# Kernel tuning notes

Hardware: AMD Instinct MI355X
Metric: run time of the kernel (lower is better)

Reference implementation:

```python
import jax, jax.numpy as jnp
import numpy as np

C = 256


def conv2d(x, w, b, stride=1, groups=1, pad=1):
    out = jax.lax.conv_general_dilated(
        x, w, (stride, stride), ((pad, pad), (pad, pad)),
        feature_group_count=groups,
        dimension_numbers=('NCHW', 'OIHW', 'NCHW'))
    return out + b[None, :, None, None]


def dwconv(x, dwW, dwB, pwW, pwB, stride=1):
    # YOLOX-style DWConv: depthwise 3x3 (+SiLU) then pointwise 1x1 (+SiLU); BN folded into bias.
    x = jax.nn.silu(conv2d(x, dwW, dwB, stride=stride, groups=x.shape[1], pad=1))
    return jax.nn.silu(conv2d(x, pwW, pwB, stride=1, groups=1, pad=0))


def resize_bilinear_ac(x, Ho, Wo):
    # bilinear with align_corners=True (semantics of F.upsample_bilinear)
    _, _, h, w = x.shape
    ys = jnp.linspace(0.0, h - 1.0, Ho)
    xs = jnp.linspace(0.0, w - 1.0, Wo)
    y0 = jnp.floor(ys).astype(jnp.int32); y1 = jnp.minimum(y0 + 1, h - 1)
    x0 = jnp.floor(xs).astype(jnp.int32); x1 = jnp.minimum(x0 + 1, w - 1)
    wy = (ys - y0)[None, None, :, None]
    wx = (xs - x0)[None, None, None, :]
    rows = x[:, :, y0, :] * (1.0 - wy) + x[:, :, y1, :] * wy
    return rows[:, :, :, x0] * (1.0 - wx) + rows[:, :, :, x1] * wx


def h_sigmoid(x):
    return jnp.clip(x + 3.0, 0.0, 6.0) / 6.0


def attn_branch(fea, aw, ab):
    # AdaptiveAvgPool2d(1) -> 1x1 conv (C->1) -> ReLU, shape [B,1,1,1]
    m = fea.mean((2, 3))                              # [B,C]
    a = jax.nn.relu(m @ aw.reshape(1, -1).T + ab)     # [B,1]
    return a[:, :, None, None]


def maxpool3x3(x):
    # 3x3 spatial max pool, stride 1, pad 1 (-inf padding like torch MaxPool)
    return jax.lax.reduce_window(x, -jnp.inf, jax.lax.max,
                                 (1, 1, 3, 3), (1, 1, 1, 1),
                                 ((0, 0), (0, 0), (1, 1), (1, 1)))


def fuse(branches, aw, ab):
    # attention-weight each branch, max over branches, then 3x3 spatial max
    # (equals MaxPool3d(kernel=(n_branch,3,3), pad=(0,1,1)) on stacked tensor)
    weighted = jnp.stack([f * h_sigmoid(attn_branch(f, aw, ab)) for f in branches])
    return maxpool3x3(weighted.max(0))


def dyrelu(x, w1, b1, w2, b2):
    # DyHead DYReLU with lambda_a=1.0 (=> *2), init_a=[1,0], init_b=[0,0]
    y = x.mean((2, 3))                                # [B,C]
    y = jax.nn.relu(y @ w1.T + b1)
    y = h_sigmoid(y @ w2.T + b2)                      # [B,4C]
    a1, bb1, a2, bb2 = jnp.split(y, 4, axis=1)
    a1 = (a1 - 0.5) * 2.0 + 1.0
    a2 = (a2 - 0.5) * 2.0
    bb1 = bb1 - 0.5
    bb2 = bb2 - 0.5
    e = lambda t: t[:, :, None, None]
    return jnp.maximum(x * e(a1) + e(bb1), x * e(a2) + e(bb2))


def setup_inputs() -> dict:
    key = jax.random.key(0)
    ks = jax.random.split(key, 12)
    B = 8
    inp = {
        'x0': jax.random.normal(ks[0], (B, C, 64, 64), jnp.float32),
        'x1': jax.random.normal(ks[1], (B, C, 32, 32), jnp.float32),
        'x2': jax.random.normal(ks[2], (B, C, 16, 16), jnp.float32),
        # 9 DWConvs (3 per level); weights init N(0, 0.01), biases zero per init_weights
        'dw_w': jax.random.normal(ks[3], (9, C, 1, 3, 3), jnp.float32) * 0.01,
        'dw_b': jnp.zeros((9, C), jnp.float32),
        'pw_w': jax.random.normal(ks[4], (9, C, C, 1, 1), jnp.float32) * 0.01,
        'pw_b': jnp.zeros((9, C), jnp.float32),
        'attn_w': jax.random.normal(ks[5], (1, C, 1, 1), jnp.float32) * 0.01,
        'attn_b': jnp.zeros((1,), jnp.float32),
        # DYReLU FCs: squeeze = C // 4
        'fc1_w': jax.random.normal(ks[6], (C // 4, C), jnp.float32) * 0.01,
        'fc1_b': jnp.zeros((C // 4,), jnp.float32),
        'fc2_w': jax.random.normal(ks[7], (4 * C, C // 4), jnp.float32) * 0.01,
        'fc2_b': jnp.zeros((4 * C,), jnp.float32),
    }
    return inp


def reference(x0, x1, x2, dw_w, dw_b, pw_w, pw_b, attn_w, attn_b,
              fc1_w, fc1_b, fc2_w, fc2_b):
    dc = lambda i, x, s=1: dwconv(x, dw_w[i], dw_b[i], pw_w[i], pw_b[i], stride=s)

    def level(branches):
        return dyrelu(fuse(branches, attn_w, attn_b), fc1_w, fc1_b, fc2_w, fc2_b)

    # level 0: own conv + upsampled next level (both use DyConv[3*0+1], as in source)
    b0 = [dc(1, x0), resize_bilinear_ac(dc(1, x1), x0.shape[2], x0.shape[3])]
    # level 1: own + stride-2 conv of prev + upsampled next
    b1 = [dc(4, x1), dc(5, x0, 2), resize_bilinear_ac(dc(4, x2), x1.shape[2], x1.shape[3])]
    # level 2 (last): own + stride-2 conv of prev
    b2 = [dc(7, x2), dc(8, x1, 2)]
    return (level(b0), level(b1), level(b2))
```

## Files before the change

### kernel.cpp

```cpp
#include <hip/hip_runtime.h>

#define BB 8
#define CC 256

typedef __attribute__((ext_vector_type(8))) short short8;
typedef __attribute__((ext_vector_type(4))) float f32x4;

__device__ __forceinline__ float silu_f(float v){ return v / (1.f + expf(-v)); }
__device__ __forceinline__ float hsig_f(float v){ return fminf(fmaxf(v + 3.f, 0.f), 6.f) * (1.f/6.f); }
__device__ __forceinline__ unsigned short f2bf(float f){
  unsigned int u = __float_as_uint(f);
  unsigned int r = u + 0x7fffu + ((u >> 16) & 1u);
  return (unsigned short)(r >> 16);
}
__device__ __forceinline__ float bf2f(unsigned short u){ return __uint_as_float(((unsigned int)u)<<16); }

struct DwG {
  const float* in;
  const float* w1a; const float* b1a; unsigned short* o1a;
  const float* w1b; const float* b1b; unsigned short* o1b;
  const float* w2;  const float* b2;  unsigned short* o2;
  int blocks;
};
struct DwPrepArgs {
  DwG g[3];
  const float* pw_w; unsigned short* wbf;
  float* wtab32; float* wtab16; float* zeros;
};

template<int C> struct RowT { float v[C+2]; };

template<int C>
__device__ __forceinline__ void loadRow(const float* rp, bool valid, bool hasL, bool hasR, RowT<C>& r){
  if (!valid){
    #pragma unroll
    for (int i=0;i<C+2;++i) r.v[i]=0.f;
    return;
  }
  r.v[0] = hasL ? rp[-1] : 0.f;
  #pragma unroll
  for (int q=0;q<C/4;++q){
    float4 f = *(const float4*)(rp + q*4);
    r.v[1+q*4+0]=f.x; r.v[1+q*4+1]=f.y; r.v[1+q*4+2]=f.z; r.v[1+q*4+3]=f.w;
  }
  r.v[C+1] = hasR ? rp[C] : 0.f;
}

template<int C>
__device__ __forceinline__ void conv1row(const RowT<C>& ra, const RowT<C>& rb, const RowT<C>& rc,
                                         const float* w9, float bias, unsigned short* dst){
  #pragma unroll
  for (int j=0;j<C;++j){
    float a = bias
      + w9[0]*ra.v[j] + w9[1]*ra.v[j+1] + w9[2]*ra.v[j+2]
      + w9[3]*rb.v[j] + w9[4]*rb.v[j+1] + w9[5]*rb.v[j+2]
      + w9[6]*rc.v[j] + w9[7]*rc.v[j+1] + w9[8]*rc.v[j+2];
    dst[j] = f2bf(silu_f(a));
  }
}

template<int C>
__device__ __forceinline__ void conv1rowS2(const RowT<C>& ra, const RowT<C>& rb, const RowT<C>& rc,
                                           const float* w9, float bias, unsigned short* dst){
  #pragma unroll
  for (int jj=0;jj<C/2;++jj){
    float a = bias
      + w9[0]*ra.v[2*jj] + w9[1]*ra.v[2*jj+1] + w9[2]*ra.v[2*jj+2]
      + w9[3]*rb.v[2*jj] + w9[4]*rb.v[2*jj+1] + w9[5]*rb.v[2*jj+2]
      + w9[6]*rc.v[2*jj] + w9[7]*rc.v[2*jj+1] + w9[8]*rc.v[2*jj+2];
    dst[jj] = f2bf(silu_f(a));
  }
}

template<int LWO, int RO, int P>
__device__ __forceinline__ void writeFrag(const unsigned short* sbuf, unsigned short* outBase,
                                          int cg, int tid){
  constexpr int WO = 1<<LWO;
  constexpr int iters = (RO*WO*8)/256;
  #pragma unroll
  for (int h=0; h<iters; ++h){
    int jc = h*256 + tid;
    int lp = jc & 15, c8 = (jc>>4)&7, ptl = jc>>7;
    int pl = ptl*16 + lp;
    int rowl = pl >> LWO, col = pl & (WO-1);
    const unsigned short* sp = sbuf + ((size_t)(c8*8)*RO + rowl)*P + col;
    unsigned int e0 = sp[0*RO*P], e1 = sp[1*RO*P], e2 = sp[2*RO*P], e3 = sp[3*RO*P];
    unsigned int e4 = sp[4*RO*P], e5 = sp[5*RO*P], e6 = sp[6*RO*P], e7 = sp[7*RO*P];
    uint4 v;
    v.x = e0 | (e1<<16); v.y = e2 | (e3<<16); v.z = e4 | (e5<<16); v.w = e6 | (e7<<16);
    size_t off = (size_t)ptl*4096 + (size_t)(cg*2 + (c8>>2))*512 + (c8&3)*128 + lp*8;
    *(uint4*)(outBase + off) = v;
  }
}

template<int LW, int R, int N1, bool S2>
__device__ void dw_group(const DwG& g, int bid, unsigned short* sm){
  constexpr int W = 1<<LW;
  constexpr int C = W/4;
  constexpr int P1 = W + 4;
  constexpr int P2 = W/2 + 4;
  const int tid = threadIdx.x;
  const int ch = tid >> 2, ct = tid & 3, c0 = ct*C;
  const int cg = bid & 3;
  int rest = bid >> 2;
  const int NR = W / R;
  const int b = rest / NR, rb = rest % NR, r0 = rb * R;

  const float* ip = g.in + ((size_t)b*CC + cg*64 + ch) * (W*W);
  const int chg = cg*64 + ch;
  float w1a[9], w1b[9], w2[9];
  float bs1a = g.b1a[chg], bs1b = 0.f, bs2 = 0.f;
  #pragma unroll
  for (int k=0;k<9;++k) w1a[k] = g.w1a[chg*9+k];
  if (N1==2){
    bs1b = g.b1b[chg];
    #pragma unroll
    for (int k=0;k<9;++k) w1b[k] = g.w1b[chg*9+k];
  }
  if (S2){
    bs2 = g.b2[chg];
    #pragma unroll
    for (int k=0;k<9;++k) w2[k] = g.w2[chg*9+k];
  }

  unsigned short* s1a = sm;
  unsigned short* s1b = sm + (size_t)64*R*P1;
  unsigned short* s2b = sm + (size_t)N1*64*R*P1;

  RowT<C> RA, RB, RC;
  const bool hasL = (c0 > 0), hasR = (c0 + C < W);
  {
    int ry = r0-1; loadRow<C>(ip + ry*W + c0, ry>=0 && ry<W, hasL, hasR, RA);
    ry = r0;       loadRow<C>(ip + ry*W + c0, ry>=0 && ry<W, hasL, hasR, RB);
    ry = r0+1;     loadRow<C>(ip + ry*W + c0, ry>=0 && ry<W, hasL, hasR, RC);
  }
  #pragma unroll
  for (int y=0; y<R; ++y){
    const RowT<C>& ra  = (y%3==0)?RA:((y%3==1)?RB:RC);
    const RowT<C>& rbm = (y%3==0)?RB:((y%3==1)?RC:RA);
    const RowT<C>& rc  = (y%3==0)?RC:((y%3==1)?RA:RB);
    conv1row<C>(ra, rbm, rc, w1a, bs1a, s1a + ((size_t)ch*R + y)*P1 + c0);
    if (N1==2) conv1row<C>(ra, rbm, rc, w1b, bs1b, s1b + ((size_t)ch*R + y)*P1 + c0);
    if (S2 && (y%2==0))
      conv1rowS2<C>(ra, rbm, rc, w2, bs2, s2b + ((size_t)ch*(R/2) + y/2)*P2 + c0/2);
    if (y < R-1){
      RowT<C>& dst = (y%3==0)?RA:((y%3==1)?RB:RC);
      int ry = r0 + y + 2;
      loadRow<C>(ip + ry*W + c0, ry>=0 && ry<W, hasL, hasR, dst);
    }
  }
  __syncthreads();

  {
    unsigned short* ob = g.o1a + ((size_t)b*(W*W) + r0*W)*256;
    writeFrag<LW, R, P1>(s1a, ob, cg, tid);
  }
  if (N1==2){
    unsigned short* ob = g.o1b + ((size_t)b*(W*W) + r0*W)*256;
    writeFrag<LW, R, P1>(s1b, ob, cg, tid);
  }
  if (S2){
    unsigned short* ob = g.o2 + ((size_t)b*((W/2)*(W/2)) + (r0/2)*(W/2))*256;
    writeFrag<LW-1, R/2, P2>(s2b, ob, cg, tid);
  }
}

__device__ float accw(int yi, int Ho, int Hi){
  float sc = (float)(Hi-1)/(float)(Ho-1);
  float a = 0.f;
  for (int yo=0; yo<Ho; ++yo){
    float ys = yo*sc; int y0 = (int)ys; float w = ys - y0; int y1 = min(y0+1, Hi-1);
    if (y0==yi) a += 1.f - w;
    if (y1==yi) a += w;
  }
  return a;
}

__global__ __launch_bounds__(256) void dw_kernel(DwPrepArgs A){
  __shared__ unsigned short smem[22016];
  int bid = blockIdx.x;
  if (bid < 832){
    int gi = 0;
    while (bid >= A.g[gi].blocks){ bid -= A.g[gi].blocks; ++gi; }
    if (gi == 0)      dw_group<6,4,1,true >(A.g[0], bid, smem);
    else if (gi == 1) dw_group<5,4,2,true >(A.g[1], bid, smem);
    else              dw_group<4,8,2,false>(A.g[2], bid, smem);
    return;
  }
  int idx = (bid - 832)*256 + threadIdx.x;
  const int T = 5*65536;
  if (idx < T){
    const int widx[5] = {1,4,5,7,8};
    int slot = idx >> 16, r = idx & 65535;
    int ct = r>>12, s=(r>>9)&7, g=(r>>7)&3, lr=(r>>3)&15, e=r&7;
    int co = ct*16+lr, k = s*32+g*8+e;
    A.wbf[idx] = f2bf(A.pw_w[(size_t)widx[slot]*65536 + co*256 + k]);
  } else if (idx < T+1024){
    int p = idx - T; int y=p>>5, x=p&31;
    A.wtab32[p] = accw(y,64,32)*accw(x,64,32);
  } else if (idx < T+1280){
    int p = idx - T - 1024; int y=p>>4, x=p&15;
    A.wtab16[p] = accw(y,32,16)*accw(x,32,16);
  } else if (idx < T+1280+20480){
    A.zeros[idx - T - 1280] = 0.f;
  }
}

struct PwT { const unsigned short* in; const unsigned short* w; const float* bias;
             unsigned short* out; const float* wtab; float norm; int HW; int blocks; int slot; };
struct PwArgs { PwT t[7]; };

__global__ __launch_bounds__(256) void pw_kernel(PwArgs A, float* __restrict__ means){
  __shared__ unsigned short cs[64*136];
  __shared__ float smean[64];
  int bid = blockIdx.x; int ti = 0;
  while (bid >= A.t[ti].blocks){ bid -= A.t[ti].blocks; ++ti; }
  PwT t = A.t[ti];
  const int nbx = t.HW >> 7;
  const int b  = bid / (nbx*4);
  const int r  = bid % (nbx*4);
  const int co0 = (r & 3) * 64;
  const int p0  = (r >> 2) * 128;
  const int tid = threadIdx.x;
  const int wid = tid >> 6, l = tid & 63;
  const int wm = wid >> 1, wn = wid & 1;
  const int lr = l & 15, g = l >> 4;

  if (tid < 64) smean[tid] = 0.f;

  const unsigned short* wbase = t.w + ((co0 + wm*32) >> 4)*4096 + l*8;
  const unsigned short* bbase = t.in + (size_t)b*t.HW*256 + ((p0 + wn*64) >> 4)*4096 + l*8;

  f32x4 acc[2][4] = {};
  #pragma unroll
  for (int s=0;s<8;++s){
    short8 av[2], bv[4];
    #pragma unroll
    for (int m=0;m<2;++m) av[m] = *(const short8*)(wbase + m*4096 + s*512);
    #pragma unroll
    for (int n=0;n<4;++n) bv[n] = *(const short8*)(bbase + n*4096 + s*512);
    #pragma unroll
    for (int m=0;m<2;++m){
      #pragma unroll
      for (int n=0;n<4;++n){
        acc[m][n] = __builtin_amdgcn_mfma_f32_16x16x32_bf16(av[m], bv[n], acc[m][n], 0,0,0);
      }
    }
  }

  float wgt[4];
  #pragma unroll
  for (int n=0;n<4;++n){
    int p = p0 + wn*64 + n*16 + lr;
    wgt[n] = t.wtab ? t.wtab[p] : 1.f;
  }

  __syncthreads();
  #pragma unroll
  for (int m=0;m<2;++m){
    #pragma unroll
    for (int rg=0;rg<4;++rg){
      int col = wm*32 + m*16 + g*4 + rg;
      float bias = t.bias[co0 + col];
      unsigned short* sp = cs + (size_t)col*136 + wn*64 + lr;
      float s = 0.f;
      #pragma unroll
      for (int n=0;n<4;++n){
        float v = silu_f(acc[m][n][rg] + bias);
        sp[n*16] = f2bf(v);
        s += v * wgt[n];
      }
      s += __shfl_xor(s, 1);
      s += __shfl_xor(s, 2);
      s += __shfl_xor(s, 4);
      s += __shfl_xor(s, 8);
      if (lr == 0) atomicAdd(&smean[col], s);
    }
  }
  __syncthreads();
  if (tid < 64){
    atomicAdd(&means[(size_t)t.slot*2048 + b*256 + co0 + tid], smean[tid] * t.norm);
  }
  #pragma unroll
  for (int h=0; h<4; ++h){
    int jc = h*256 + tid;
    int col = jc >> 4, pq = jc & 15;
    uint4 v = *(const uint4*)(cs + (size_t)col*136 + pq*8);
    unsigned short* op = t.out + ((size_t)(b*256 + co0 + col))*t.HW + p0 + pq*8;
    *(uint4*)op = v;
  }
}

struct FpT { const unsigned short* uA; const unsigned short* uB; const unsigned short* uUp;
             unsigned short* fea; int iA, iB, iUp, blocks; float norm; int lvl; };
struct FpArgs { FpT t[3]; };

template<int H, int LW, int SLAB, bool HASB, bool HASU, int HUP>
__device__ void fusepool_body(const FpT& t, int bid,
                              const float* __restrict__ means,
                              const float* __restrict__ atw, const float* __restrict__ atb,
                              float* __restrict__ feaMean, float* __restrict__ Vs){
  constexpr int W = 1 << LW;
  constexpr int P = W + 2;
  const int tid = threadIdx.x;
  const int bc = bid & 2047, si = bid >> 11;
  const int b = bc >> 8;
  const int r0 = si * SLAB;
  const unsigned short* pA = t.uA + (size_t)bc*H*W;
  const unsigned short* pB = HASB ? t.uB + (size_t)bc*H*W : nullptr;
  const unsigned short* pU = HASU ? t.uUp + (size_t)bc*HUP*HUP : nullptr;

  __shared__ float red4[4][3];
  __shared__ float atnL[3];
  {
    float awv = (tid < 256) ? atw[tid] : 0.f;
    float s0 = means[(size_t)t.iA*2048 + b*256 + tid] * awv;
    float s1 = HASB ? means[(size_t)t.iB*2048 + b*256 + tid] * awv : 0.f;
    float s2 = HASU ? means[(size_t)t.iUp*2048 + b*256 + tid] * awv : 0.f;
    #pragma unroll
    for (int off=32; off; off>>=1){
      s0 += __shfl_down(s0, off);
      if (HASB) s1 += __shfl_down(s1, off);
      if (HASU) s2 += __shfl_down(s2, off);
    }
    int wid = tid >> 6;
    if ((tid & 63) == 0){ red4[wid][0]=s0; red4[wid][1]=s1; red4[wid][2]=s2; }
    __syncthreads();
    if (tid == 0){
      float ab0 = atb[0];
      atnL[0] = hsig_f(fmaxf(red4[0][0]+red4[1][0]+red4[2][0]+red4[3][0] + ab0, 0.f));
      if (HASB) atnL[1] = hsig_f(fmaxf(red4[0][1]+red4[1][1]+red4[2][1]+red4[3][1] + ab0, 0.f));
      if (HASU) atnL[2] = hsig_f(fmaxf(red4[0][2]+red4[1][2]+red4[2][2]+red4[3][2] + ab0, 0.f));
    }
    __syncthreads();
  }
  const float wA = atnL[0];
  const float wB = HASB ? atnL[1] : 0.f;
  const float wU = HASU ? atnL[2] : 0.f;
  const float SC = HASU ? (float)(HUP-1)/(float)(H-1) : 0.f;

  for (int r=tid; r<SLAB+2; r+=256){ Vs[r*P] = -INFINITY; Vs[r*P + W+1] = -INFINITY; }

  constexpr int NQ = (SLAB+2)*(W/4);
  for (int q=tid; q<NQ; q+=256){
    int row = q >> (LW-2);
    int xq = (q & ((W/4)-1)) << 2;
    int y = r0 - 1 + row;
    float v0=-INFINITY, v1=-INFINITY, v2=-INFINITY, v3=-INFINITY;
    if (y >= 0 && y < H){
      int ro = y*W + xq;
      ushort4 a4 = *(const ushort4*)(pA + ro);
      v0 = bf2f(a4.x)*wA; v1 = bf2f(a4.y)*wA; v2 = bf2f(a4.z)*wA; v3 = bf2f(a4.w)*wA;
      if (HASB){
        ushort4 b4 = *(const ushort4*)(pB + ro);
        v0 = fmaxf(v0, bf2f(b4.x)*wB); v1 = fmaxf(v1, bf2f(b4.y)*wB);
        v2 = fmaxf(v2, bf2f(b4.z)*wB); v3 = fmaxf(v3, bf2f(b4.w)*wB);
      }
      if (HASU){
        float ys = y*SC; int y0 = (int)ys; float fy = ys - y0; int y1 = min(y0+1, HUP-1);
        const unsigned short* pu0 = pU + y0*HUP;
        const unsigned short* pu1 = pU + y1*HUP;
        float gy = 1.f - fy;
        #pragma unroll
        for (int j=0;j<4;++j){
          int x = xq + j;
          float xs = x*SC; int x0 = (int)xs; float fx = xs - x0; int x1 = min(x0+1, HUP-1);
          float gx = 1.f - fx;
          float ra = bf2f(pu0[x0])*gx + bf2f(pu0[x1])*fx;
          float rb = bf2f(pu1[x0])*gx + bf2f(pu1[x1])*fx;
          float uv = (ra*gy + rb*fy) * wU;
          if (j==0) v0 = fmaxf(v0, uv);
          else if (j==1) v1 = fmaxf(v1, uv);
          else if (j==2) v2 = fmaxf(v2, uv);
          else v3 = fmaxf(v3, uv);
        }
      }
    }
    float* vr = Vs + row*P + 1 + xq;
    vr[0]=v0; vr[1]=v1; vr[2]=v2; vr[3]=v3;
  }
  __syncthreads();

  float sum = 0.f;
  constexpr int NO = SLAB*(W/4);
  unsigned short* fb = t.fea + (size_t)bc*H*W + r0*W;
  for (int q=tid; q<NO; q+=256){
    int row = q >> (LW-2);
    int x4 = (q & ((W/4)-1)) << 2;
    const float* rp0 = Vs + row*P + x4;
    const float* rp1 = rp0 + P;
    const float* rp2 = rp1 + P;
    float c0,c1,c2,c3,c4,c5, m0,m1,m2,m3;
    c0=rp0[0]; c1=rp0[1]; c2=rp0[2]; c3=rp0[3]; c4=rp0[4]; c5=rp0[5];
    m0 = fmaxf(fmaxf(c0,c1),c2);
    m1 = fmaxf(fmaxf(c1,c2),c3);
    m2 = fmaxf(fmaxf(c2,c3),c4);
    m3 = fmaxf(fmaxf(c3,c4),c5);
    c0=rp1[0]; c1=rp1[1]; c2=rp1[2]; c3=rp1[3]; c4=rp1[4]; c5=rp1[5];
    m0 = fmaxf(m0, fmaxf(fmaxf(c0,c1),c2));
    m1 = fmaxf(m1, fmaxf(fmaxf(c1,c2),c3));
    m2 = fmaxf(m2, fmaxf(fmaxf(c2,c3),c4));
    m3 = fmaxf(m3, fmaxf(fmaxf(c3,c4),c5));
    c0=rp2[0]; c1=rp2[1]; c2=rp2[2]; c3=rp2[3]; c4=rp2[4]; c5=rp2[5];
    m0 = fmaxf(m0, fmaxf(fmaxf(c0,c1),c2));
    m1 = fmaxf(m1, fmaxf(fmaxf(c1,c2),c3));
    m2 = fmaxf(m2, fmaxf(fmaxf(c2,c3),c4));
    m3 = fmaxf(m3, fmaxf(fmaxf(c3,c4),c5));
    ushort4 o; o.x=f2bf(m0); o.y=f2bf(m1); o.z=f2bf(m2); o.w=f2bf(m3);
    *(ushort4*)(fb + row*W + x4) = o;
    sum += m0+m1+m2+m3;
  }
  #pragma unroll
  for (int off=32; off; off>>=1) sum += __shfl_down(sum, off);
  __shared__ float red[4];
  if ((tid & 63) == 0) red[tid >> 6] = sum;
  __syncthreads();
  if (tid == 0)
    atomicAdd(&feaMean[t.lvl*2048 + bc], (red[0]+red[1]+red[2]+red[3]) * t.norm);
}

__global__ __launch_bounds__(256) void fusepool_kernel(FpArgs A,
                                                       const float* __restrict__ means,
                                                       const float* __restrict__ atw,
                                                       const float* __restrict__ atb,
                                                       float* __restrict__ feaMean){
  __shared__ float Vs[34*66];
  int bid = blockIdx.x; int ti = 0;
  while (bid >= A.t[ti].blocks){ bid -= A.t[ti].blocks; ++ti; }
  if (ti == 0)      fusepool_body<64,6,32,false,true,32>(A.t[0], bid, means, atw, atb, feaMean, Vs);
  else if (ti == 1) fusepool_body<32,5,32,true, true,16>(A.t[1], bid, means, atw, atb, feaMean, Vs);
  else              fusepool_body<16,4,16,true,false, 2>(A.t[2], bid, means, atw, atb, feaMean, Vs);
}

__global__ __launch_bounds__(256) void fc_kernel(const float* __restrict__ feaMean,
                                                 const float* __restrict__ w1, const float* __restrict__ b1,
                                                 const float* __restrict__ w2, const float* __restrict__ b2,
                                                 float* __restrict__ coef){
  int lb = blockIdx.x;
  const float* m = feaMean + (size_t)lb*CC;
  __shared__ float sm[CC];
  __shared__ float sy[64];
  sm[threadIdx.x] = m[threadIdx.x];
  __syncthreads();
  if (threadIdx.x < 64){
    float s = b1[threadIdx.x];
    const float* wr = w1 + (size_t)threadIdx.x*CC;
    for (int k=0;k<CC;++k) s += wr[k]*sm[k];
    sy[threadIdx.x] = fmaxf(s, 0.f);
  }
  __syncthreads();
  for (int j = threadIdx.x; j < 1024; j += 256){
    float s = b2[j];
    const float* wr = w2 + (size_t)j*64;
    for (int k=0;k<64;++k) s += wr[k]*sy[k];
    float y = hsig_f(s);
    int seg = j >> 8;
    float o;
    if (seg==0)      o = (y-0.5f)*2.f + 1.f;
    else if (seg==1) o = y - 0.5f;
    else if (seg==2) o = (y-0.5f)*2.f;
    else             o = y - 0.5f;
    coef[(size_t)lb*1024 + j] = o;
  }
}

struct ApT { const unsigned short* fea; const float* coefL; float* out; int lhw; int blocks; };
struct ApArgs { ApT t[3]; };

__global__ __launch_bounds__(256) void apply_kernel(ApArgs A){
  int bid = blockIdx.x; int ti = 0;
  while (bid >= A.t[ti].blocks){ bid -= A.t[ti].blocks; ++ti; }
  ApT t = A.t[ti];
  int e0 = bid*2048 + threadIdx.x*8;
  int bc = e0 >> t.lhw;
  int b = bc >> 8, c = bc & 255;
  const float* cf = t.coefL + (size_t)b*1024;
  float a1 = cf[c], bb1 = cf[256+c], a2 = cf[512+c], bb2 = cf[768+c];
  uint4 xv = *(const uint4*)(t.fea + e0);
  float x0 = bf2f((unsigned short)(xv.x & 0xffff)), x1 = bf2f((unsigned short)(xv.x >> 16));
  float x2 = bf2f((unsigned short)(xv.y & 0xffff)), x3 = bf2f((unsigned short)(xv.y >> 16));
  float x4 = bf2f((unsigned short)(xv.z & 0xffff)), x5 = bf2f((unsigned short)(xv.z >> 16));
  float x6 = bf2f((unsigned short)(xv.w & 0xffff)), x7 = bf2f((unsigned short)(xv.w >> 16));
  float4 o0, o1;
  o0.x = fmaxf(x0*a1 + bb1, x0*a2 + bb2);
  o0.y = fmaxf(x1*a1 + bb1, x1*a2 + bb2);
  o0.z = fmaxf(x2*a1 + bb1, x2*a2 + bb2);
  o0.w = fmaxf(x3*a1 + bb1, x3*a2 + bb2);
  o1.x = fmaxf(x4*a1 + bb1, x4*a2 + bb2);
  o1.y = fmaxf(x5*a1 + bb1, x5*a2 + bb2);
  o1.z = fmaxf(x6*a1 + bb1, x6*a2 + bb2);
  o1.w = fmaxf(x7*a1 + bb1, x7*a2 + bb2);
  *(float4*)(t.out + e0) = o0;
  *(float4*)(t.out + e0 + 4) = o1;
}

extern "C" void kernel_launch(void* const* d_in, const int* in_sizes, int n_in,
                              void* d_out, int out_size, void* d_ws, size_t ws_size,
                              hipStream_t stream) {
  const float* x0    = (const float*)d_in[0];
  const float* x1    = (const float*)d_in[1];
  const float* x2    = (const float*)d_in[2];
  const float* dw_w  = (const float*)d_in[3];
  const float* dw_b  = (const float*)d_in[4];
  const float* pw_w  = (const float*)d_in[5];
  const float* pw_b  = (const float*)d_in[6];
  const float* atw   = (const float*)d_in[7];
  const float* atb   = (const float*)d_in[8];
  const float* fc1w  = (const float*)d_in[9];
  const float* fc1b  = (const float*)d_in[10];
  const float* fc2w  = (const float*)d_in[11];
  const float* fc2b  = (const float*)d_in[12];
  float* out = (float*)d_out;

  const size_t A64 = (size_t)BB*CC*64*64;
  const size_t A32 = (size_t)BB*CC*32*32;
  const size_t A16 = (size_t)BB*CC*16*16;

  unsigned short* us = (unsigned short*)d_ws;
  unsigned short* bA = us;
  unsigned short* bB = bA + A64;
  unsigned short* bC = bB + A32;
  unsigned short* bD = bC + A32;
  unsigned short* bE = bD + A32;
  unsigned short* bF = bE + A16;
  unsigned short* bG = bF + A16;
  unsigned short* uA = bG + A16;
  unsigned short* uB = uA + A64;
  unsigned short* uC = uB + A32;
  unsigned short* uD = uC + A32;
  unsigned short* uE = uD + A32;
  unsigned short* uF = uE + A16;
  unsigned short* uG = uF + A16;
  unsigned short* fe0 = uG + A16;
  unsigned short* fe1 = fe0 + A64;
  unsigned short* fe2 = fe1 + A32;
  unsigned short* wbf = fe2 + A16;
  float* fb      = (float*)(wbf + 5*65536);
  float* wtab32  = fb;
  float* wtab16  = wtab32 + 1024;
  float* means   = wtab16 + 256;
  float* feaMean = means + 7*2048;
  float* attnW   = feaMean + 3*2048;
  float* coef    = attnW + 64;

  const float* W1 = dw_w + 1*CC*9; const float* B1 = dw_b + 1*CC;
  const float* W4 = dw_w + 4*CC*9; const float* B4 = dw_b + 4*CC;
  const float* W5 = dw_w + 5*CC*9; const float* B5 = dw_b + 5*CC;
  const float* W7 = dw_w + 7*CC*9; const float* B7 = dw_b + 7*CC;
  const float* W8 = dw_w + 8*CC*9; const float* B8 = dw_b + 8*CC;

  {
    DwPrepArgs DA;
    DA.g[0] = {x0, W1,B1,bA,  nullptr,nullptr,nullptr,  W5,B5,bD,  512};
    DA.g[1] = {x1, W1,B1,bB,  W4,B4,bC,                 W8,B8,bG,  256};
    DA.g[2] = {x2, W4,B4,bE,  W7,B7,bF,                 nullptr,nullptr,nullptr, 64};
    DA.pw_w = pw_w; DA.wbf = wbf; DA.wtab32 = wtab32; DA.wtab16 = wtab16; DA.zeros = means;
    dw_kernel<<<832 + 1365, 256, 0, stream>>>(DA);
  }

  {
    PwArgs A;
    A.t[0] = {bA, wbf + 0*65536, pw_b + 1*CC, uA, nullptr, 1.f/4096.f, 4096, 1024, 0};
    A.t[1] = {bB, wbf + 0*65536, pw_b + 1*CC, uB, wtab32,  1.f/4096.f, 1024, 256, 1};
    A.t[2] = {bC, wbf + 1*65536, pw_b + 4*CC, uC, nullptr, 1.f/1024.f, 1024, 256, 2};
    A.t[3] = {bD, wbf + 2*65536, pw_b + 5*CC, uD, nullptr, 1.f/1024.f, 1024, 256, 3};
    A.t[4] = {bE, wbf + 1*65536, pw_b + 4*CC, uE, wtab16,  1.f/1024.f, 256,  64, 4};
    A.t[5] = {bF, wbf + 3*65536, pw_b + 7*CC, uF, nullptr, 1.f/256.f,  256,  64, 5};
    A.t[6] = {bG, wbf + 4*65536, pw_b + 8*CC, uG, nullptr, 1.f/256.f,  256,  64, 6};
    pw_kernel<<<1984, 256, 0, stream>>>(A, means);
  }

  {
    FpArgs F;
    F.t[0] = {uA, nullptr, uB,      fe0, 0,-1, 1, 4096, 1.f/4096.f, 0};
    F.t[1] = {uC, uD,      uE,      fe1, 2, 3, 4, 2048, 1.f/1024.f, 1};
    F.t[2] = {uF, uG,      nullptr, fe2, 5, 6,-1, 2048, 1.f/256.f,  2};
    fusepool_kernel<<<8192, 256, 0, stream>>>(F, means, atw, atb, feaMean);
  }

  fc_kernel<<<24, 256, 0, stream>>>(feaMean, fc1w, fc1b, fc2w, fc2b, coef);

  {
    ApArgs P;
    P.t[0] = {fe0, coef + 0*8192, out,             12, 4096};
    P.t[1] = {fe1, coef + 1*8192, out + A64,       10, 1024};
    P.t[2] = {fe2, coef + 2*8192, out + A64 + A32,  8, 256};
    apply_kernel<<<5376, 256, 0, stream>>>(P);
  }
}
```

Before: 128.5 us.

## Split depthwise conv blocks into 32-channel groups with 8 threads per channel row

The depthwise-conv stage now assigns 32 channels per block instead of 64, with 8 threads sharing each row instead of 4. This doubles the block count and halves shared memory per block, aiming for better occupancy and lower per-thread register pressure. The fragment writer is rewritten to pack the 32-channel half into the same blocked bf16 output layout. The cost is more halo loads per row and narrower per-thread work; for W=16, C=2 falls back to scalar loads.

```diff
diff --git a/kernel.cpp b/kernel.cpp
--- a/kernel.cpp
+++ b/kernel.cpp
@@ -38,10 +38,15 @@
     return;
   }
   r.v[0] = hasL ? rp[-1] : 0.f;
-  #pragma unroll
-  for (int q=0;q<C/4;++q){
-    float4 f = *(const float4*)(rp + q*4);
-    r.v[1+q*4+0]=f.x; r.v[1+q*4+1]=f.y; r.v[1+q*4+2]=f.z; r.v[1+q*4+3]=f.w;
+  if constexpr (C >= 4){
+    #pragma unroll
+    for (int q=0;q<C/4;++q){
+      float4 f = *(const float4*)(rp + q*4);
+      r.v[1+q*4+0]=f.x; r.v[1+q*4+1]=f.y; r.v[1+q*4+2]=f.z; r.v[1+q*4+3]=f.w;
+    }
+  } else {
+    #pragma unroll
+    for (int i=0;i<C;++i) r.v[1+i] = rp[i];
   }
   r.v[C+1] = hasR ? rp[C] : 0.f;
 }
@@ -73,41 +78,44 @@
 }
 
 template<int LWO, int RO, int P>
-__device__ __forceinline__ void writeFrag(const unsigned short* sbuf, unsigned short* outBase,
-                                          int cg, int tid){
+__device__ __forceinline__ void writeFrag32(const unsigned short* sbuf, unsigned short* outBase,
+                                            int cg, int tid){
   constexpr int WO = 1<<LWO;
-  constexpr int iters = (RO*WO*8)/256;
+  constexpr int total = RO*WO*4;
+  constexpr int iters = (total + 255)/256;
   #pragma unroll
   for (int h=0; h<iters; ++h){
     int jc = h*256 + tid;
-    int lp = jc & 15, c8 = (jc>>4)&7, ptl = jc>>7;
-    int pl = ptl*16 + lp;
-    int rowl = pl >> LWO, col = pl & (WO-1);
-    const unsigned short* sp = sbuf + ((size_t)(c8*8)*RO + rowl)*P + col;
-    unsigned int e0 = sp[0*RO*P], e1 = sp[1*RO*P], e2 = sp[2*RO*P], e3 = sp[3*RO*P];
-    unsigned int e4 = sp[4*RO*P], e5 = sp[5*RO*P], e6 = sp[6*RO*P], e7 = sp[7*RO*P];
-    uint4 v;
-    v.x = e0 | (e1<<16); v.y = e2 | (e3<<16); v.z = e4 | (e5<<16); v.w = e6 | (e7<<16);
-    size_t off = (size_t)ptl*4096 + (size_t)(cg*2 + (c8>>2))*512 + (c8&3)*128 + lp*8;
-    *(uint4*)(outBase + off) = v;
+    if (jc < total){
+      int lp = jc & 15, c4 = (jc>>4)&3, pt = jc>>6;
+      int pl = pt*16 + lp;
+      int rowl = pl >> LWO, col = pl & (WO-1);
+      const unsigned short* sp = sbuf + ((size_t)(c4*8)*RO + rowl)*P + col;
+      unsigned int e0 = sp[0*RO*P], e1 = sp[1*RO*P], e2 = sp[2*RO*P], e3 = sp[3*RO*P];
+      unsigned int e4 = sp[4*RO*P], e5 = sp[5*RO*P], e6 = sp[6*RO*P], e7 = sp[7*RO*P];
+      uint4 v;
+      v.x = e0 | (e1<<16); v.y = e2 | (e3<<16); v.z = e4 | (e5<<16); v.w = e6 | (e7<<16);
+      size_t off = (size_t)pt*4096 + (size_t)cg*512 + c4*128 + lp*8;
+      *(uint4*)(outBase + off) = v;
+    }
   }
 }
 
 template<int LW, int R, int N1, bool S2>
-__device__ void dw_group(const DwG& g, int bid, unsigned short* sm){
+__device__ void dw_group32(const DwG& g, int bid, unsigned short* sm){
   constexpr int W = 1<<LW;
-  constexpr int C = W/4;
+  constexpr int C = W/8;
   constexpr int P1 = W + 4;
   constexpr int P2 = W/2 + 4;
   const int tid = threadIdx.x;
-  const int ch = tid >> 2, ct = tid & 3, c0 = ct*C;
-  const int cg = bid & 3;
-  int rest = bid >> 2;
+  const int ch = tid >> 3, ct = tid & 7, c0 = ct*C;
+  const int cg = bid & 7;
+  int rest = bid >> 3;
   const int NR = W / R;
   const int b = rest / NR, rb = rest % NR, r0 = rb * R;
 
-  const float* ip = g.in + ((size_t)b*CC + cg*64 + ch) * (W*W);
-  const int chg = cg*64 + ch;
+  const float* ip = g.in + ((size_t)b*CC + cg*32 + ch) * (W*W);
+  const int chg = cg*32 + ch;
   float w1a[9], w1b[9], w2[9];
   float bs1a = g.b1a[chg], bs1b = 0.f, bs2 = 0.f;
   #pragma unroll
@@ -124,8 +132,8 @@
   }
 
   unsigned short* s1a = sm;
-  unsigned short* s1b = sm + (size_t)64*R*P1;
-  unsigned short* s2b = sm + (size_t)N1*64*R*P1;
+  unsigned short* s1b = sm + (size_t)32*R*P1;
+  unsigned short* s2b = sm + (size_t)N1*32*R*P1;
 
   RowT<C> RA, RB, RC;
   const bool hasL = (c0 > 0), hasR = (c0 + C < W);
@@ -153,15 +161,15 @@
 
   {
     unsigned short* ob = g.o1a + ((size_t)b*(W*W) + r0*W)*256;
-    writeFrag<LW, R, P1>(s1a, ob, cg, tid);
+    writeFrag32<LW, R, P1>(s1a, ob, cg, tid);
   }
   if (N1==2){
     unsigned short* ob = g.o1b + ((size_t)b*(W*W) + r0*W)*256;
-    writeFrag<LW, R, P1>(s1b, ob, cg, tid);
+    writeFrag32<LW, R, P1>(s1b, ob, cg, tid);
   }
   if (S2){
     unsigned short* ob = g.o2 + ((size_t)b*((W/2)*(W/2)) + (r0/2)*(W/2))*256;
-    writeFrag<LW-1, R/2, P2>(s2b, ob, cg, tid);
+    writeFrag32<LW-1, R/2, P2>(s2b, ob, cg, tid);
   }
 }
 
@@ -177,17 +185,17 @@
 }
 
 __global__ __launch_bounds__(256) void dw_kernel(DwPrepArgs A){
-  __shared__ unsigned short smem[22016];
+  __shared__ unsigned short smem[11008];
   int bid = blockIdx.x;
-  if (bid < 832){
+  if (bid < 1664){
     int gi = 0;
     while (bid >= A.g[gi].blocks){ bid -= A.g[gi].blocks; ++gi; }
-    if (gi == 0)      dw_group<6,4,1,true >(A.g[0], bid, smem);
-    else if (gi == 1) dw_group<5,4,2,true >(A.g[1], bid, smem);
-    else              dw_group<4,8,2,false>(A.g[2], bid, smem);
+    if (gi == 0)      dw_group32<6,4,1,true >(A.g[0], bid, smem);
+    else if (gi == 1) dw_group32<5,4,2,true >(A.g[1], bid, smem);
+    else              dw_group32<4,8,2,false>(A.g[2], bid, smem);
     return;
   }
-  int idx = (bid - 832)*256 + threadIdx.x;
+  int idx = (bid - 1664)*256 + threadIdx.x;
   const int T = 5*65536;
   if (idx < T){
     const int widx[5] = {1,4,5,7,8};
@@ -551,11 +559,11 @@
 
   {
     DwPrepArgs DA;
-    DA.g[0] = {x0, W1,B1,bA,  nullptr,nullptr,nullptr,  W5,B5,bD,  512};
-    DA.g[1] = {x1, W1,B1,bB,  W4,B4,bC,                 W8,B8,bG,  256};
-    DA.g[2] = {x2, W4,B4,bE,  W7,B7,bF,                 nullptr,nullptr,nullptr, 64};
+    DA.g[0] = {x0, W1,B1,bA,  nullptr,nullptr,nullptr,  W5,B5,bD,  1024};
+    DA.g[1] = {x1, W1,B1,bB,  W4,B4,bC,                 W8,B8,bG,  512};
+    DA.g[2] = {x2, W4,B4,bE,  W7,B7,bF,                 nullptr,nullptr,nullptr, 128};
     DA.pw_w = pw_w; DA.wbf = wbf; DA.wtab32 = wtab32; DA.wtab16 = wtab16; DA.zeros = means;
-    dw_kernel<<<832 + 1365, 256, 0, stream>>>(DA);
+    dw_kernel<<<1664 + 1365, 256, 0, stream>>>(DA);
   }
 
   {
```

New measurement: 127.3 us. About the same (-0.9%).
